# Performance work log

Measured on AMD Instinct MI355X. Metric: run time of the kernel, lower is better.

Reference implementation:

```python
import jax, jax.numpy as jnp
import numpy as np

D_MODEL, D_STATE, EXPAND = 1024, 16, 2
D_INNER = D_MODEL * EXPAND
BATCH, SEQ = 4, 2048
DT = 0.1

def setup_inputs() -> dict:
    key = jax.random.key(0)
    ks = jax.random.split(key, 12)
    s = 0.02
    inp = {
        "x": jax.random.normal(ks[0], (BATCH, SEQ, D_MODEL), jnp.float32),
        "B_mod": jax.random.normal(ks[1], (BATCH, D_STATE), jnp.float32) * 0.1,
        "C_mod": jax.random.normal(ks[2], (BATCH, D_STATE), jnp.float32) * 0.1,
        "W_in": jax.random.normal(ks[3], (D_MODEL, 2 * D_INNER), jnp.float32) * s,
        "b_in": jnp.zeros((2 * D_INNER,), jnp.float32),
        "conv_w": jax.random.normal(ks[4], (D_INNER, 1, 3), jnp.float32) * 0.3,
        "conv_b": jnp.zeros((D_INNER,), jnp.float32),
        "A_log": jnp.tile(jnp.log(jnp.arange(1, D_STATE + 1, dtype=jnp.float32))[None, :], (D_INNER, 1)),
        "D": jnp.ones((D_INNER,), jnp.float32),
        "W_B": jax.random.normal(ks[5], (D_INNER, D_STATE), jnp.float32) * s,
        "b_B": jnp.zeros((D_STATE,), jnp.float32),
        "W_C": jax.random.normal(ks[6], (D_INNER, D_STATE), jnp.float32) * s,
        "b_C": jnp.zeros((D_STATE,), jnp.float32),
        "W_out": jax.random.normal(ks[7], (D_INNER, D_MODEL), jnp.float32) * s,
        "b_out": jnp.zeros((D_MODEL,), jnp.float32),
    }
    return inp

def _silu(v):
    return v * jax.nn.sigmoid(v)

def reference(x, B_mod, C_mod, W_in, b_in, conv_w, conv_b, A_log, D, W_B, b_B, W_C, b_C, W_out, b_out):
    # in_proj + split + gate
    xr = x @ W_in + b_in                      # (B, L, 2*D_INNER)
    x_ssm, x_res = jnp.split(xr, 2, axis=-1)
    x_ssm = _silu(x_ssm)
    # depthwise conv1d, kernel 3, padding 1
    xc = jnp.transpose(x_ssm, (0, 2, 1))      # (B, C, L)
    xc = jax.lax.conv_general_dilated(
        xc, conv_w, window_strides=(1,), padding=[(1, 1)],
        dimension_numbers=("NCH", "OIH", "NCH"), feature_group_count=D_INNER)
    xc = xc + conv_b[None, :, None]
    x_ssm = jnp.transpose(xc, (0, 2, 1))      # (B, L, D_INNER)
    # SSM params
    A = -jnp.exp(A_log)                       # (D_INNER, D_STATE)
    A_bar = jnp.exp(A * DT)
    B = x_ssm @ W_B + b_B + B_mod[:, None, :] # (B, L, D_STATE)
    C = x_ssm @ W_C + b_C + C_mod[:, None, :]
    # sequential scan over time
    def step(h, inp):
        xt, Bt, Ct = inp                      # (B,D_INNER), (B,S), (B,S)
        h = A_bar[None] * h + xt[:, :, None] * Bt[:, None, :]
        yt = jnp.einsum("bds,bs->bd", h, Ct)
        return h, yt
    h0 = jnp.zeros((x.shape[0], D_INNER, D_STATE), x.dtype)
    xs = (jnp.moveaxis(x_ssm, 1, 0), jnp.moveaxis(B, 1, 0), jnp.moveaxis(C, 1, 0))
    _, ys = jax.lax.scan(step, h0, xs)        # (L, B, D_INNER)
    y = jnp.moveaxis(ys, 0, 1) + D[None, None, :] * x_ssm
    y = y * _silu(x_res)
    return y @ W_out + b_out
```

## Files before the change

### kernel.cpp

```cpp
#include <hip/hip_runtime.h>
#include <stdint.h>

#define D_MODEL 1024
#define D_STATE 16
#define D_INNER 2048
#define BATCH   4
#define SEQ     2048
#define ML      (BATCH*SEQ)
#define CH      64
#define NCHUNK  (SEQ/CH)
#define KSEG    8

typedef unsigned short u16;
typedef u16   u16x8  __attribute__((ext_vector_type(8)));
typedef short s16x8  __attribute__((ext_vector_type(8)));
typedef float f32x4  __attribute__((ext_vector_type(4)));

__device__ __forceinline__ float b2f(u16 u){
  union { uint32_t i; float f; } v; v.i = ((uint32_t)u) << 16; return v.f;
}
__device__ __forceinline__ u16 f2b(float f){
  uint32_t x = __float_as_uint(f);
  return (u16)((x + 0x7fffu + ((x >> 16) & 1u)) >> 16);
}
__device__ __forceinline__ float silu_f(float v){
  return v / (1.f + __expf(-v));
}
__device__ __forceinline__ void gl_lds16(const void* gp, void* lp){
  __builtin_amdgcn_global_load_lds(
      (const __attribute__((address_space(1))) void*)gp,
      (__attribute__((address_space(3))) void*)lp, 16, 0, 0);
}

__global__ __launch_bounds__(256) void prep_k(const float* __restrict__ W_in,
                                              const float* __restrict__ W_out,
                                              const float* __restrict__ x,
                                              const float* __restrict__ W_B,
                                              const float* __restrict__ W_C,
                                              u16* __restrict__ Wt_in,
                                              u16* __restrict__ Wt_out,
                                              u16* __restrict__ xbf,
                                              u16* __restrict__ Wt_bc){
  __shared__ float tile[32][33];
  int bb = blockIdx.x;
  if (bb < 6144) {
    const float* in; u16* out; int R, C, bx, by;
    if (bb < 4096) { in = W_in;  out = Wt_in;  R = 1024; C = 4096;
                     bx = (bb & 127) * 32; by = (bb >> 7) * 32; }
    else { bb -= 4096; in = W_out; out = Wt_out; R = 2048; C = 1024;
                     bx = (bb & 31) * 32; by = (bb >> 5) * 32; }
    int tx = threadIdx.x & 31, ty = threadIdx.x >> 5;
    #pragma unroll
    for (int i = 0; i < 32; i += 8)
      tile[ty + i][tx] = in[(size_t)(by + ty + i) * C + bx + tx];
    __syncthreads();
    #pragma unroll
    for (int i = 0; i < 32; i += 8)
      out[(size_t)(bx + ty + i) * R + by + tx] = f2b(tile[tx][ty + i]);
  } else if (bb < 10240) {
    bb -= 6144;
    size_t i = ((size_t)bb * 256 + threadIdx.x) * 8;
    f32x4 a = *(const f32x4*)(x + i);
    f32x4 b = *(const f32x4*)(x + i + 4);
    u16x8 o;
    #pragma unroll
    for (int j = 0; j < 4; ++j){ o[j] = f2b(a[j]); o[4+j] = f2b(b[j]); }
    *(u16x8*)(xbf + i) = o;
  } else {
    bb -= 10240;
    int n = bb >> 3;
    int k = (bb & 7) * 256 + threadIdx.x;
    const float* src = (n < 16) ? W_B : W_C;
    Wt_bc[(size_t)n * D_INNER + k] = f2b(src[(size_t)k * 16 + (n & 15)]);
  }
}

#define G1_K  1024
#define G1_NT (G1_K/64)

__global__ __launch_bounds__(512, 2) void gemm1_k(const u16* __restrict__ A,
                                                  const u16* __restrict__ Bt,
                                                  const float* __restrict__ bias,
                                                  u16* __restrict__ out0,
                                                  u16* __restrict__ out1){
  __shared__ __align__(16) u16 ldsAll[256*264];
  u16* ldsA = ldsAll;
  u16* ldsB = ldsAll + 4*8192;

  const int bid = blockIdx.x;
  const int xcd = bid & 7, t2 = bid >> 3;
  const int n0 = (xcd*2 + (t2 & 1)) * 256;
  const int m0 = (t2 >> 1) * 256;

  const int tid  = threadIdx.x;
  const int wave = tid >> 6, lane = tid & 63;
  const int wr = wave >> 2;
  const int wc = wave & 3;
  const int lrow = lane & 15;
  const int q    = lane >> 4;

  const int cx0  = ((q ^ (lrow & 7)) << 3);
  const int cx1  = cx0 ^ 32;
  const int arow = lrow * 64;

  const int srow = lane >> 3;
  const int scol = (((lane & 7) ^ (lane >> 3)) << 3);

  auto stageA = [&](int buf, int h, int k0){
    const u16* s = A + (size_t)(m0 + h*128 + wave*16 + srow) * G1_K + k0 + scol;
    u16* d = ldsA + (buf*2 + h)*8192 + wave*1024;
    gl_lds16(s,                  d);
    gl_lds16(s + (size_t)8*G1_K, d + 512);
  };
  auto stageB = [&](int buf, int h, int k0){
    const u16* s = Bt + (size_t)(n0 + h*128 + wave*16 + srow) * G1_K + k0 + scol;
    u16* d = ldsB + (buf*2 + h)*8192 + wave*1024;
    gl_lds16(s,                  d);
    gl_lds16(s + (size_t)8*G1_K, d + 512);
  };

  f32x4 acc[8][4];
  #pragma unroll
  for (int i = 0; i < 8; ++i)
    #pragma unroll
    for (int j = 0; j < 4; ++j) acc[i][j] = (f32x4){0.f,0.f,0.f,0.f};

  s16x8 aA[2][2], aB[2][2];
  s16x8 bX[4][2], bY[4][2];

  #define READ_AQ(dst, Q, nb)                                            \
    { const u16* p_ = ldsA + ((nb)*2 + wr)*8192 + (Q)*2048 + arow;       \
      dst[0][0] = *(const s16x8*)(p_ + cx0);                             \
      dst[0][1] = *(const s16x8*)(p_ + cx1);                             \
      dst[1][0] = *(const s16x8*)(p_ + 1024 + cx0);                      \
      dst[1][1] = *(const s16x8*)(p_ + 1024 + cx1); }
  #define READ_B8(dst, nb)                                               \
    { const u16* p_ = ldsB + ((nb)*2 + (wc>>1))*8192 + (wc&1)*4096 + arow; \
      _Pragma("unroll")                                                  \
      for (int nj_ = 0; nj_ < 4; ++nj_){                                 \
        dst[nj_][0] = *(const s16x8*)(p_ + nj_*1024 + cx0);              \
        dst[nj_][1] = *(const s16x8*)(p_ + nj_*1024 + cx1); } }
  #define MFMA_Q(Q, AF, BF)                                              \
    { _Pragma("unroll")                                                  \
      for (int nj_ = 0; nj_ < 4; ++nj_){                                 \
        _Pragma("unroll")                                                \
        for (int kk_ = 0; kk_ < 2; ++kk_){                               \
          acc[2*(Q)][nj_]   = __builtin_amdgcn_mfma_f32_16x16x32_bf16(AF[0][kk_], BF[nj_][kk_], acc[2*(Q)][nj_],   0,0,0); \
          acc[2*(Q)+1][nj_] = __builtin_amdgcn_mfma_f32_16x16x32_bf16(AF[1][kk_], BF[nj_][kk_], acc[2*(Q)+1][nj_], 0,0,0); } } }

  stageA(0,0,0); stageA(0,1,0); stageB(0,0,0); stageB(0,1,0);
  stageB(1,0,64); stageB(1,1,64);
  asm volatile("s_waitcnt vmcnt(4)" ::: "memory");
  __builtin_amdgcn_s_barrier();
  __builtin_amdgcn_sched_barrier(0);
  READ_B8(bX, 0);
  READ_AQ(aA, 0, 0);

  auto tile_body = [&](int tt, int buf, s16x8 (&bC)[4][2], s16x8 (&bN)[4][2]){
    const int k1 = (tt+1 < G1_NT ? tt+1 : G1_NT-1) * 64;
    const int k2 = (tt+2 < G1_NT ? tt+2 : G1_NT-1) * 64;
    const int nb = buf ^ 1;

    READ_AQ(aB, 1, buf);
    stageA(nb, 1, k1);
    stageA(nb, 0, k1);
    __builtin_amdgcn_s_barrier();
    asm volatile("s_waitcnt lgkmcnt(4)" ::: "memory");
    __builtin_amdgcn_sched_barrier(0);
    __builtin_amdgcn_s_setprio(1);
    MFMA_Q(0, aA, bC);
    __builtin_amdgcn_s_setprio(0);
    __builtin_amdgcn_s_barrier();

    READ_AQ(aA, 2, buf);
    stageB(buf, 0, k2);
    __builtin_amdgcn_s_barrier();
    asm volatile("s_waitcnt lgkmcnt(4)" ::: "memory");
    __builtin_amdgcn_sched_barrier(0);
    __builtin_amdgcn_s_setprio(1);
    MFMA_Q(1, aB, bC);
    __builtin_amdgcn_s_setprio(0);
    __builtin_amdgcn_s_barrier();

    READ_AQ(aB, 3, buf);
    stageB(buf, 1, k2);
    __builtin_amdgcn_s_barrier();
    asm volatile("s_waitcnt lgkmcnt(4)" ::: "memory");
    __builtin_amdgcn_sched_barrier(0);
    __builtin_amdgcn_s_setprio(1);
    MFMA_Q(2, aA, bC);
    __builtin_amdgcn_s_setprio(0);
    __builtin_amdgcn_s_barrier();

    asm volatile("s_waitcnt vmcnt(4)" ::: "memory");
    __builtin_amdgcn_s_barrier();
    __builtin_amdgcn_sched_barrier(0);
    READ_B8(bN, nb);
    READ_AQ(aA, 0, nb);
    asm volatile("s_waitcnt lgkmcnt(12)" ::: "memory");
    __builtin_amdgcn_sched_barrier(0);
    __builtin_amdgcn_s_setprio(1);
    MFMA_Q(3, aB, bC);
    __builtin_amdgcn_s_setprio(0);
    __builtin_amdgcn_s_barrier();
  };

  for (int tt2 = 0; tt2 < G1_NT; tt2 += 2) {
    tile_body(tt2,     0, bX, bY);
    tile_body(tt2 + 1, 1, bY, bX);
  }

  asm volatile("s_waitcnt vmcnt(0)" ::: "memory");
  __syncthreads();

  #pragma unroll
  for (int nj = 0; nj < 4; ++nj) {
    const int colg = n0 + wc*64 + nj*16 + lrow;
    const float bv = bias[colg];
    const int coll = wc*64 + nj*16 + lrow;
    #pragma unroll
    for (int mi = 0; mi < 8; ++mi) {
      #pragma unroll
      for (int r = 0; r < 4; ++r) {
        const int rowl = wr*128 + mi*16 + q*4 + r;
        ldsAll[rowl*264 + coll] = f2b(silu_f(acc[mi][nj][r] + bv));
      }
    }
  }
  __syncthreads();

  u16* op = (n0 < D_INNER) ? out0 : out1;
  const int colbase = n0 & (D_INNER - 1);
  #pragma unroll
  for (int it = 0; it < 16; ++it) {
    const int f   = it*512 + tid;
    const int row = f >> 5;
    const int ch  = f & 31;
    u16x8 v = *(const u16x8*)(ldsAll + row*264 + ch*8);
    *(u16x8*)(op + (size_t)(m0 + row)*D_INNER + colbase + ch*8) = v;
  }
  #undef READ_AQ
  #undef READ_B8
  #undef MFMA_Q
}

template<int MODE>
__global__ __launch_bounds__(256) void gemm_bt(const u16* __restrict__ A,
                                               const u16* __restrict__ Bt,
                                               const float* __restrict__ bias,
                                               u16* __restrict__ out0,
                                               u16* __restrict__ out1,
                                               float* __restrict__ outf,
                                               int M, int N, int K, int n_per_xcd){
  __shared__ __align__(16) u16 Asb[2][128*32];
  __shared__ __align__(16) u16 Bsb[2][128*32];
  const int bid = blockIdx.x;
  const int xcd = bid & 7, t2 = bid >> 3;
  const int n0 = (xcd * n_per_xcd + (t2 % n_per_xcd)) * 128;
  const int m0 = (t2 / n_per_xcd) * 128;
  const int t    = threadIdx.x;
  const int wave = t >> 6, lane = t & 63;
  const int wm   = (wave >> 1) * 64, wn = (wave & 1) * 64;
  const int lrow = lane & 15, kq = (lane >> 4) * 8;
  const int srow = lane >> 2;
  const int scol = (lane & 3) * 8;

  f32x4 acc[4][4];
  #pragma unroll
  for (int i = 0; i < 4; ++i)
    #pragma unroll
    for (int j = 0; j < 4; ++j)
      acc[i][j] = (f32x4){0.f, 0.f, 0.f, 0.f};

  auto stage = [&](int buf, int k0){
    #pragma unroll
    for (int i = 0; i < 2; ++i) {
      int R0 = (wave*2 + i) * 16;
      gl_lds16(&A [(size_t)(m0 + R0 + srow)*K + k0 + scol], &Asb[buf][R0*32]);
      gl_lds16(&Bt[(size_t)(n0 + R0 + srow)*K + k0 + scol], &Bsb[buf][R0*32]);
    }
  };

  const int KT = K >> 5;
  stage(0, 0);
  __syncthreads();
  for (int kt = 0; kt < KT; ++kt) {
    const int cur = kt & 1;
    if (kt + 1 < KT) stage(1 - cur, (kt + 1) * 32);
    s16x8 af[4], bfr[4];
    #pragma unroll
    for (int i = 0; i < 4; ++i) af[i]  = *(const s16x8*)&Asb[cur][(wm + i*16 + lrow)*32 + kq];
    #pragma unroll
    for (int j = 0; j < 4; ++j) bfr[j] = *(const s16x8*)&Bsb[cur][(wn + j*16 + lrow)*32 + kq];
    #pragma unroll
    for (int i = 0; i < 4; ++i)
      #pragma unroll
      for (int j = 0; j < 4; ++j)
        acc[i][j] = __builtin_amdgcn_mfma_f32_16x16x32_bf16(af[i], bfr[j], acc[i][j], 0, 0, 0);
    __syncthreads();
  }

  const int Nh = N >> 1;
  #pragma unroll
  for (int i = 0; i < 4; ++i) {
    #pragma unroll
    for (int j = 0; j < 4; ++j) {
      int col = n0 + wn + j*16 + lrow;
      float bv = bias[col];
      #pragma unroll
      for (int r = 0; r < 4; ++r) {
        int row = m0 + wm + i*16 + (lane >> 4)*4 + r;
        float v = acc[i][j][r] + bv;
        if (MODE == 0) {
          outf[(size_t)row * N + col] = v;
        } else {
          float s = silu_f(v);
          if (col < Nh) out0[(size_t)row * Nh + col]        = f2b(s);
          else          out1[(size_t)row * Nh + (col - Nh)] = f2b(s);
        }
      }
    }
  }
}

__global__ __launch_bounds__(256) void bc_gemm_k(const u16* __restrict__ xs,
                                                 const float* __restrict__ conv_w,
                                                 const float* __restrict__ conv_b,
                                                 const u16* __restrict__ Wt,
                                                 float* __restrict__ partial){
  __shared__ __align__(16) u16 Rsb[130*40];
  __shared__ __align__(16) u16 Asb[128*40];
  __shared__ __align__(16) u16 Wsb[32*40];
  const int kseg = blockIdx.x;
  const int m0   = blockIdx.y * 128;
  const int t    = threadIdx.x;
  const int wave = t >> 6, lane = t & 63;
  const int wm   = wave * 32;
  const int lrow = lane & 15, kq = (lane >> 4) * 8;
  const bool zfirst = (m0 & (SEQ-1)) == 0;
  const bool zlast  = ((m0+128) & (SEQ-1)) == 0;
  const int ccol = t & 31, r0c = (t >> 5) * 16;

  f32x4 acc[2][2];
  #pragma unroll
  for (int i = 0; i < 2; ++i)
    #pragma unroll
    for (int j = 0; j < 2; ++j)
      acc[i][j] = (f32x4){0.f, 0.f, 0.f, 0.f};

  const int kbase = kseg * (D_INNER / KSEG);
  for (int ks = 0; ks < (D_INNER / KSEG); ks += 32) {
    int k0 = kbase + ks;
    if (t < 128) {
      int f = t * 8;
      int r = f >> 5, c = f & 31;
      *(u16x8*)&Wsb[r*40 + c] = *(const u16x8*)&Wt[(size_t)r*D_INNER + k0 + c];
    }
    #pragma unroll
    for (int i = 0; i < 3; ++i) {
      int idx = i*256 + t;
      if (idx < 520) {
        int r = idx >> 2, c = (idx & 3) * 8;
        u16x8 v = (u16x8){0,0,0,0,0,0,0,0};
        bool zero = (r == 0 && zfirst) || (r == 129 && zlast);
        if (!zero)
          v = *(const u16x8*)&xs[(size_t)(m0 - 1 + r)*D_INNER + k0 + c];
        *(u16x8*)&Rsb[r*40 + c] = v;
      }
    }
    __syncthreads();
    {
      const int dcol = k0 + ccol;
      const float cw0 = conv_w[dcol*3], cw1 = conv_w[dcol*3+1], cw2 = conv_w[dcol*3+2];
      const float cbv = conv_b[dcol];
      #pragma unroll
      for (int r = 0; r < 16; ++r) {
        int rr = r0c + r;
        float v = cw0 * b2f(Rsb[rr*40 + ccol])
                + cw1 * b2f(Rsb[(rr+1)*40 + ccol])
                + cw2 * b2f(Rsb[(rr+2)*40 + ccol]) + cbv;
        Asb[rr*40 + ccol] = f2b(v);
      }
    }
    __syncthreads();
    s16x8 af[2], wf[2];
    #pragma unroll
    for (int i = 0; i < 2; ++i) af[i] = *(const s16x8*)&Asb[(wm + i*16 + lrow)*40 + kq];
    #pragma unroll
    for (int j = 0; j < 2; ++j) wf[j] = *(const s16x8*)&Wsb[(j*16 + lrow)*40 + kq];
    #pragma unroll
    for (int i = 0; i < 2; ++i)
      #pragma unroll
      for (int j = 0; j < 2; ++j)
        acc[i][j] = __builtin_amdgcn_mfma_f32_16x16x32_bf16(af[i], wf[j], acc[i][j], 0, 0, 0);
    __syncthreads();
  }

  #pragma unroll
  for (int i = 0; i < 2; ++i)
    #pragma unroll
    for (int j = 0; j < 2; ++j)
      #pragma unroll
      for (int r = 0; r < 4; ++r) {
        int row = m0 + wm + i*16 + (lane >> 4)*4 + r;
        int col = j*16 + lrow;
        partial[((size_t)kseg * ML + row) * 32 + col] = acc[i][j][r];
      }
}

__global__ __launch_bounds__(256) void bc_reduce_k(const float* __restrict__ partial,
    const float* __restrict__ b_B, const float* __restrict__ B_mod,
    const float* __restrict__ b_C, const float* __restrict__ C_mod,
    float* __restrict__ Bbuf, float* __restrict__ Cbuf){
  int g = blockIdx.x * 256 + threadIdx.x;
  int row = g >> 5, col = g & 31;
  int b = row >> 11;
  float s = 0.f;
  #pragma unroll
  for (int seg = 0; seg < KSEG; ++seg)
    s += partial[(size_t)seg * ML * 32 + g];
  if (col < 16) Bbuf[(size_t)row*16 + col]      = s + b_B[col]      + B_mod[b*16 + col];
  else          Cbuf[(size_t)row*16 + col - 16] = s + b_C[col - 16] + C_mod[b*16 + col - 16];
}

__global__ __launch_bounds__(256) void state_k(const u16* __restrict__ xs,
    const float* __restrict__ conv_w, const float* __restrict__ conv_b,
    const float* __restrict__ Bbuf, const float* __restrict__ A_log,
    float* __restrict__ hend){
  int c = blockIdx.x, db = blockIdx.y, b = blockIdx.z;
  int d = db*256 + threadIdx.x;

  float Abar[16];
  #pragma unroll
  for (int s = 0; s < 16; ++s)
    Abar[s] = __expf(-0.1f * __expf(A_log[d*16 + s]));
  float h[16];
  #pragma unroll
  for (int s = 0; s < 16; ++s) h[s] = 0.f;

  const float w0 = conv_w[d*3], w1 = conv_w[d*3+1], w2 = conv_w[d*3+2], cb = conv_b[d];
  size_t base = (size_t)b * SEQ * D_INNER + (size_t)c * CH * D_INNER + d;
  const float* Br = Bbuf + ((size_t)b * SEQ + (size_t)c * CH) * 16;
  const int l0 = c * CH;

  float xm = (l0 > 0) ? b2f(xs[base - D_INNER]) : 0.f;
  float x0 = b2f(xs[base]);
  float xp = b2f(xs[base + D_INNER]);
  float Bc[16];
  #pragma unroll
  for (int s = 0; s < 16; ++s) Bc[s] = Br[s];

  for (int l = 0; l < CH; ++l){
    float xq = 0.f;
    if (l0 + l + 2 < SEQ) xq = b2f(xs[base + (size_t)(l+2)*D_INNER]);
    float Bl[16];
    #pragma unroll
    for (int s = 0; s < 16; ++s) Bl[s] = Bc[s];
    if (l < CH-1){
      #pragma unroll
      for (int s = 0; s < 16; ++s) Bc[s] = Br[(l+1)*16 + s];
    }
    float xc = w0*xm + w1*x0 + w2*xp + cb;
    #pragma unroll
    for (int s = 0; s < 16; ++s)
      h[s] = Abar[s]*h[s] + xc*Bl[s];
    xm = x0; x0 = xp; xp = xq;
  }
  float* hp = hend + (((size_t)(b*NCHUNK + c))*D_INNER + d)*16;
  #pragma unroll
  for (int q = 0; q < 4; ++q)
    *(f32x4*)(hp + q*4) = (f32x4){h[q*4], h[q*4+1], h[q*4+2], h[q*4+3]};
}

__global__ __launch_bounds__(256) void prefix_k(const float* __restrict__ hend,
    const float* __restrict__ A_log, float* __restrict__ hin){
  int g = blockIdx.x*256 + threadIdx.x;
  int s = g & 15;
  int d = (g >> 4) & (D_INNER-1);
  int b = g >> 15;
  float decay = __expf(-0.1f * (float)CH * __expf(A_log[d*16 + s]));
  size_t stride = (size_t)D_INNER * 16;
  const float* he = hend + (size_t)b*NCHUNK*stride + (size_t)d*16 + s;
  float*       hi = hin  + (size_t)b*NCHUNK*stride + (size_t)d*16 + s;
  float h = 0.f;
  for (int c0 = 0; c0 < NCHUNK; c0 += 8){
    float v[8];
    #pragma unroll
    for (int i = 0; i < 8; ++i) v[i] = he[(size_t)(c0+i)*stride];
    #pragma unroll
    for (int i = 0; i < 8; ++i){
      hi[(size_t)(c0+i)*stride] = h;
      h = decay*h + v[i];
    }
  }
}

__global__ __launch_bounds__(256) void scan2_k(const u16* __restrict__ xs,
    const u16* __restrict__ gate,
    const float* __restrict__ conv_w, const float* __restrict__ conv_b,
    const float* __restrict__ Bbuf, const float* __restrict__ Cbuf,
    const float* __restrict__ A_log, const float* __restrict__ Dp,
    const float* __restrict__ hin, u16* __restrict__ ybuf){
  int c = blockIdx.x, db = blockIdx.y, b = blockIdx.z;
  int d = db*256 + threadIdx.x;

  float Abar[16];
  #pragma unroll
  for (int s = 0; s < 16; ++s)
    Abar[s] = __expf(-0.1f * __expf(A_log[d*16 + s]));
  float h[16];
  const float* hp = hin + (((size_t)(b*NCHUNK + c))*D_INNER + d)*16;
  #pragma unroll
  for (int q = 0; q < 4; ++q){
    f32x4 v = *(const f32x4*)(hp + q*4);
    #pragma unroll
    for (int j = 0; j < 4; ++j) h[q*4 + j] = v[j];
  }
  float Dd = Dp[d];
  const float w0 = conv_w[d*3], w1 = conv_w[d*3+1], w2 = conv_w[d*3+2], cb = conv_b[d];

  size_t base = (size_t)b * SEQ * D_INNER + (size_t)c * CH * D_INNER + d;
  const float* Br = Bbuf + ((size_t)b * SEQ + (size_t)c * CH) * 16;
  const float* Cr = Cbuf + ((size_t)b * SEQ + (size_t)c * CH) * 16;
  const int l0 = c * CH;

  float xm = (l0 > 0) ? b2f(xs[base - D_INNER]) : 0.f;
  float x0 = b2f(xs[base]);
  float xp = b2f(xs[base + D_INNER]);
  float Bc[16], Cc[16];
  #pragma unroll
  for (int s = 0; s < 16; ++s){ Bc[s] = Br[s]; Cc[s] = Cr[s]; }
  float gcur = b2f(gate[base]);

  for (int l = 0; l < CH; ++l){
    float xq = 0.f;
    if (l0 + l + 2 < SEQ) xq = b2f(xs[base + (size_t)(l+2)*D_INNER]);
    float gnext = (l < CH-1) ? b2f(gate[base + (size_t)(l+1)*D_INNER]) : 0.f;
    float Bl[16], Cl[16];
    #pragma unroll
    for (int s = 0; s < 16; ++s){ Bl[s] = Bc[s]; Cl[s] = Cc[s]; }
    if (l < CH-1){
      #pragma unroll
      for (int s = 0; s < 16; ++s){ Bc[s] = Br[(l+1)*16 + s]; Cc[s] = Cr[(l+1)*16 + s]; }
    }
    float xc = w0*xm + w1*x0 + w2*xp + cb;
    float ya[4] = {0.f, 0.f, 0.f, 0.f};
    #pragma unroll
    for (int s = 0; s < 16; ++s){
      float hv = Abar[s]*h[s] + xc*Bl[s];
      h[s] = hv;
      ya[s & 3] += hv * Cl[s];
    }
    float y = ((ya[0]+ya[1]) + (ya[2]+ya[3]) + Dd*xc) * gcur;
    ybuf[base + (size_t)l*D_INNER] = f2b(y);
    xm = x0; x0 = xp; xp = xq; gcur = gnext;
  }
}

extern "C" void kernel_launch(void* const* d_in, const int* in_sizes, int n_in,
                              void* d_out, int out_size, void* d_ws, size_t ws_size,
                              hipStream_t stream){
  const float* x      = (const float*)d_in[0];
  const float* B_mod  = (const float*)d_in[1];
  const float* C_mod  = (const float*)d_in[2];
  const float* W_in   = (const float*)d_in[3];
  const float* b_in   = (const float*)d_in[4];
  const float* conv_w = (const float*)d_in[5];
  const float* conv_b = (const float*)d_in[6];
  const float* A_log  = (const float*)d_in[7];
  const float* Dp     = (const float*)d_in[8];
  const float* W_B    = (const float*)d_in[9];
  const float* b_B    = (const float*)d_in[10];
  const float* W_C    = (const float*)d_in[11];
  const float* b_C    = (const float*)d_in[12];
  const float* W_out  = (const float*)d_in[13];
  const float* b_out  = (const float*)d_in[14];
  float* out = (float*)d_out;

  char* ws = (char*)d_ws;
  size_t off = 0;
  auto alloc = [&](size_t bytes)->char* {
    char* p = ws + off; off += (bytes + 255) & ~(size_t)255; return p;
  };
  u16* Wt_in  = (u16*)alloc((size_t)(2*D_INNER)*D_MODEL*2);
  u16* Wt_out = (u16*)alloc((size_t)D_MODEL*D_INNER*2);
  u16* xs     = (u16*)alloc((size_t)ML*D_INNER*2);
  u16* gatep  = (u16*)alloc((size_t)ML*D_INNER*2);
  u16* ybuf   = (u16*)alloc((size_t)ML*D_INNER*2);
  float* Bbuf = (float*)alloc((size_t)ML*D_STATE*4);
  float* Cbuf = (float*)alloc((size_t)ML*D_STATE*4);
  u16* xbf    = (u16*)alloc((size_t)ML*D_MODEL*2);
  float* hin  = (float*)alloc((size_t)BATCH*NCHUNK*D_INNER*16*4);
  u16* Wt_bc  = (u16*)alloc((size_t)32*D_INNER*2);
  float* hend    = (float*)xbf;
  float* partial = (float*)Wt_in;

  prep_k<<<dim3(10496), 256, 0, stream>>>(W_in, W_out, x, W_B, W_C,
                                          Wt_in, Wt_out, xbf, Wt_bc);

  gemm1_k<<<dim3(512), 512, 0, stream>>>(xbf, Wt_in, b_in, xs, gatep);

  bc_gemm_k<<<dim3(KSEG, ML/128), 256, 0, stream>>>(xs, conv_w, conv_b, Wt_bc, partial);
  bc_reduce_k<<<dim3((ML*32)/256), 256, 0, stream>>>(
      partial, b_B, B_mod, b_C, C_mod, Bbuf, Cbuf);

  state_k<<<dim3(NCHUNK, D_INNER/256, BATCH), 256, 0, stream>>>(
      xs, conv_w, conv_b, Bbuf, A_log, hend);
  prefix_k<<<dim3((BATCH*D_INNER*16)/256), 256, 0, stream>>>(hend, A_log, hin);
  scan2_k<<<dim3(NCHUNK, D_INNER/256, BATCH), 256, 0, stream>>>(
      xs, gatep, conv_w, conv_b, Bbuf, Cbuf, A_log, Dp, hin, ybuf);

  gemm_bt<0><<<dim3(512), 256, 0, stream>>>(
      ybuf, Wt_out, b_out, nullptr, nullptr, out, ML, D_MODEL, D_INNER, 1);
}
```

Measured before the change: 370.8 us.

## Replace 256x256 ping-pong in_proj GEMM with simpler 256x128 tile, higher occupancy

The in_proj GEMM kernel drops its hand-scheduled 256x256 tile with quarter-step interleaving, setprio and explicit waitcnts. It now uses a 256x128 tile with K-step 32, a plain double-buffered loop synchronised by one __syncthreads per step, and a launch bound of 4 blocks per CU. The grid doubles to 1024 blocks, and the epilogue writes the output through LDS in two halves to fit the smaller shared buffer. The aim is to hide latency through occupancy rather than manual scheduling. The cost is less reuse per tile, more barriers, and a short K-step that may expose load latency.

Result: faster. 359.0 us (-3.2%).

```diff
diff --git a/kernel.cpp b/kernel.cpp
--- a/kernel.cpp
+++ b/kernel.cpp
@@ -76,172 +76,101 @@
 }
 
 #define G1_K  1024
-#define G1_NT (G1_K/64)
-
-__global__ __launch_bounds__(512, 2) void gemm1_k(const u16* __restrict__ A,
+
+__global__ __launch_bounds__(512, 4) void gemm1_k(const u16* __restrict__ A,
                                                   const u16* __restrict__ Bt,
                                                   const float* __restrict__ bias,
                                                   u16* __restrict__ out0,
                                                   u16* __restrict__ out1){
-  __shared__ __align__(16) u16 ldsAll[256*264];
-  u16* ldsA = ldsAll;
-  u16* ldsB = ldsAll + 4*8192;
+  __shared__ __align__(16) u16 lds[24576];
+  u16* ldsA = lds;
+  u16* ldsB = lds + 16384;
 
   const int bid = blockIdx.x;
   const int xcd = bid & 7, t2 = bid >> 3;
-  const int n0 = (xcd*2 + (t2 & 1)) * 256;
-  const int m0 = (t2 >> 1) * 256;
+  const int n0 = (xcd*4 + (t2 & 3)) * 128;
+  const int m0 = (t2 >> 2) * 256;
 
   const int tid  = threadIdx.x;
   const int wave = tid >> 6, lane = tid & 63;
-  const int wr = wave >> 2;
-  const int wc = wave & 3;
+  const int wr = wave >> 1;
+  const int wn = (wave & 1) * 64;
   const int lrow = lane & 15;
   const int q    = lane >> 4;
 
-  const int cx0  = ((q ^ (lrow & 7)) << 3);
-  const int cx1  = cx0 ^ 32;
-  const int arow = lrow * 64;
-
-  const int srow = lane >> 3;
-  const int scol = (((lane & 7) ^ (lane >> 3)) << 3);
-
-  auto stageA = [&](int buf, int h, int k0){
-    const u16* s = A + (size_t)(m0 + h*128 + wave*16 + srow) * G1_K + k0 + scol;
-    u16* d = ldsA + (buf*2 + h)*8192 + wave*1024;
-    gl_lds16(s,                  d);
-    gl_lds16(s + (size_t)8*G1_K, d + 512);
+  const int cxa  = (q ^ (lrow & 3)) << 3;
+  const int srow = lane >> 2;
+  const int schunk = (((lane & 3) ^ (srow & 3)) << 3);
+
+  auto stageA = [&](int buf, int k0){
+    const u16* s = A + (size_t)(m0 + wave*32 + srow) * G1_K + k0 + schunk;
+    u16* d = ldsA + buf*8192 + wave*1024;
+    gl_lds16(s,                   d);
+    gl_lds16(s + (size_t)16*G1_K, d + 512);
   };
-  auto stageB = [&](int buf, int h, int k0){
-    const u16* s = Bt + (size_t)(n0 + h*128 + wave*16 + srow) * G1_K + k0 + scol;
-    u16* d = ldsB + (buf*2 + h)*8192 + wave*1024;
-    gl_lds16(s,                  d);
-    gl_lds16(s + (size_t)8*G1_K, d + 512);
+  auto stageB = [&](int buf, int k0){
+    const u16* s = Bt + (size_t)(n0 + wave*16 + srow) * G1_K + k0 + schunk;
+    gl_lds16(s, ldsB + buf*4096 + wave*512);
   };
 
-  f32x4 acc[8][4];
-  #pragma unroll
-  for (int i = 0; i < 8; ++i)
+  f32x4 acc[4][4];
+  #pragma unroll
+  for (int i = 0; i < 4; ++i)
     #pragma unroll
     for (int j = 0; j < 4; ++j) acc[i][j] = (f32x4){0.f,0.f,0.f,0.f};
 
-  s16x8 aA[2][2], aB[2][2];
-  s16x8 bX[4][2], bY[4][2];
-
-  #define READ_AQ(dst, Q, nb)                                            \
-    { const u16* p_ = ldsA + ((nb)*2 + wr)*8192 + (Q)*2048 + arow;       \
-      dst[0][0] = *(const s16x8*)(p_ + cx0);                             \
-      dst[0][1] = *(const s16x8*)(p_ + cx1);                             \
-      dst[1][0] = *(const s16x8*)(p_ + 1024 + cx0);                      \
-      dst[1][1] = *(const s16x8*)(p_ + 1024 + cx1); }
-  #define READ_B8(dst, nb)                                               \
-    { const u16* p_ = ldsB + ((nb)*2 + (wc>>1))*8192 + (wc&1)*4096 + arow; \
-      _Pragma("unroll")                                                  \
-      for (int nj_ = 0; nj_ < 4; ++nj_){                                 \
-        dst[nj_][0] = *(const s16x8*)(p_ + nj_*1024 + cx0);              \
-        dst[nj_][1] = *(const s16x8*)(p_ + nj_*1024 + cx1); } }
-  #define MFMA_Q(Q, AF, BF)                                              \
-    { _Pragma("unroll")                                                  \
-      for (int nj_ = 0; nj_ < 4; ++nj_){                                 \
-        _Pragma("unroll")                                                \
-        for (int kk_ = 0; kk_ < 2; ++kk_){                               \
-          acc[2*(Q)][nj_]   = __builtin_amdgcn_mfma_f32_16x16x32_bf16(AF[0][kk_], BF[nj_][kk_], acc[2*(Q)][nj_],   0,0,0); \
-          acc[2*(Q)+1][nj_] = __builtin_amdgcn_mfma_f32_16x16x32_bf16(AF[1][kk_], BF[nj_][kk_], acc[2*(Q)+1][nj_], 0,0,0); } } }
-
-  stageA(0,0,0); stageA(0,1,0); stageB(0,0,0); stageB(0,1,0);
-  stageB(1,0,64); stageB(1,1,64);
-  asm volatile("s_waitcnt vmcnt(4)" ::: "memory");
-  __builtin_amdgcn_s_barrier();
-  __builtin_amdgcn_sched_barrier(0);
-  READ_B8(bX, 0);
-  READ_AQ(aA, 0, 0);
-
-  auto tile_body = [&](int tt, int buf, s16x8 (&bC)[4][2], s16x8 (&bN)[4][2]){
-    const int k1 = (tt+1 < G1_NT ? tt+1 : G1_NT-1) * 64;
-    const int k2 = (tt+2 < G1_NT ? tt+2 : G1_NT-1) * 64;
-    const int nb = buf ^ 1;
-
-    READ_AQ(aB, 1, buf);
-    stageA(nb, 1, k1);
-    stageA(nb, 0, k1);
-    __builtin_amdgcn_s_barrier();
-    asm volatile("s_waitcnt lgkmcnt(4)" ::: "memory");
-    __builtin_amdgcn_sched_barrier(0);
-    __builtin_amdgcn_s_setprio(1);
-    MFMA_Q(0, aA, bC);
-    __builtin_amdgcn_s_setprio(0);
-    __builtin_amdgcn_s_barrier();
-
-    READ_AQ(aA, 2, buf);
-    stageB(buf, 0, k2);
-    __builtin_amdgcn_s_barrier();
-    asm volatile("s_waitcnt lgkmcnt(4)" ::: "memory");
-    __builtin_amdgcn_sched_barrier(0);
-    __builtin_amdgcn_s_setprio(1);
-    MFMA_Q(1, aB, bC);
-    __builtin_amdgcn_s_setprio(0);
-    __builtin_amdgcn_s_barrier();
-
-    READ_AQ(aB, 3, buf);
-    stageB(buf, 1, k2);
-    __builtin_amdgcn_s_barrier();
-    asm volatile("s_waitcnt lgkmcnt(4)" ::: "memory");
-    __builtin_amdgcn_sched_barrier(0);
-    __builtin_amdgcn_s_setprio(1);
-    MFMA_Q(2, aA, bC);
-    __builtin_amdgcn_s_setprio(0);
-    __builtin_amdgcn_s_barrier();
-
-    asm volatile("s_waitcnt vmcnt(4)" ::: "memory");
-    __builtin_amdgcn_s_barrier();
-    __builtin_amdgcn_sched_barrier(0);
-    READ_B8(bN, nb);
-    READ_AQ(aA, 0, nb);
-    asm volatile("s_waitcnt lgkmcnt(12)" ::: "memory");
-    __builtin_amdgcn_sched_barrier(0);
-    __builtin_amdgcn_s_setprio(1);
-    MFMA_Q(3, aB, bC);
-    __builtin_amdgcn_s_setprio(0);
-    __builtin_amdgcn_s_barrier();
-  };
-
-  for (int tt2 = 0; tt2 < G1_NT; tt2 += 2) {
-    tile_body(tt2,     0, bX, bY);
-    tile_body(tt2 + 1, 1, bY, bX);
-  }
-
-  asm volatile("s_waitcnt vmcnt(0)" ::: "memory");
+  stageA(0, 0); stageB(0, 0);
   __syncthreads();
 
-  #pragma unroll
-  for (int nj = 0; nj < 4; ++nj) {
-    const int colg = n0 + wc*64 + nj*16 + lrow;
-    const float bv = bias[colg];
-    const int coll = wc*64 + nj*16 + lrow;
-    #pragma unroll
-    for (int mi = 0; mi < 8; ++mi) {
-      #pragma unroll
-      for (int r = 0; r < 4; ++r) {
-        const int rowl = wr*128 + mi*16 + q*4 + r;
-        ldsAll[rowl*264 + coll] = f2b(silu_f(acc[mi][nj][r] + bv));
-      }
-    }
-  }
-  __syncthreads();
+  const int KT = G1_K / 32;
+  for (int kt = 0; kt < KT; ++kt) {
+    const int cur = kt & 1;
+    if (kt + 1 < KT) { stageA(1 - cur, (kt+1)*32); stageB(1 - cur, (kt+1)*32); }
+    s16x8 af[4], bf[4];
+    #pragma unroll
+    for (int mi = 0; mi < 4; ++mi)
+      af[mi] = *(const s16x8*)&ldsA[cur*8192 + (wr*64 + mi*16 + lrow)*32 + cxa];
+    #pragma unroll
+    for (int nj = 0; nj < 4; ++nj)
+      bf[nj] = *(const s16x8*)&ldsB[cur*4096 + (wn + nj*16 + lrow)*32 + cxa];
+    #pragma unroll
+    for (int mi = 0; mi < 4; ++mi)
+      #pragma unroll
+      for (int nj = 0; nj < 4; ++nj)
+        acc[mi][nj] = __builtin_amdgcn_mfma_f32_16x16x32_bf16(af[mi], bf[nj], acc[mi][nj], 0,0,0);
+    __syncthreads();
+  }
 
   u16* op = (n0 < D_INNER) ? out0 : out1;
   const int colbase = n0 & (D_INNER - 1);
   #pragma unroll
-  for (int it = 0; it < 16; ++it) {
-    const int f   = it*512 + tid;
-    const int row = f >> 5;
-    const int ch  = f & 31;
-    u16x8 v = *(const u16x8*)(ldsAll + row*264 + ch*8);
-    *(u16x8*)(op + (size_t)(m0 + row)*D_INNER + colbase + ch*8) = v;
-  }
-  #undef READ_AQ
-  #undef READ_B8
-  #undef MFMA_Q
+  for (int h = 0; h < 2; ++h) {
+    __syncthreads();
+    if ((wr >> 1) == h) {
+      const int rbase = (wr & 1) * 64;
+      #pragma unroll
+      for (int nj = 0; nj < 4; ++nj) {
+        const int col = wn + nj*16 + lrow;
+        const float bv = bias[n0 + col];
+        #pragma unroll
+        for (int mi = 0; mi < 4; ++mi) {
+          #pragma unroll
+          for (int r = 0; r < 4; ++r) {
+            const int row = rbase + mi*16 + q*4 + r;
+            lds[row*136 + col] = f2b(silu_f(acc[mi][nj][r] + bv));
+          }
+        }
+      }
+    }
+    __syncthreads();
+    #pragma unroll
+    for (int it = 0; it < 4; ++it) {
+      const int f = it*512 + tid;
+      const int row = f >> 4, ch = f & 15;
+      u16x8 v = *(const u16x8*)&lds[row*136 + ch*8];
+      *(u16x8*)(op + (size_t)(m0 + h*128 + row)*D_INNER + colbase + ch*8) = v;
+    }
+  }
 }
 
 template<int MODE>
@@ -598,7 +527,7 @@
   prep_k<<<dim3(10496), 256, 0, stream>>>(W_in, W_out, x, W_B, W_C,
                                           Wt_in, Wt_out, xbf, Wt_bc);
 
-  gemm1_k<<<dim3(512), 512, 0, stream>>>(xbf, Wt_in, b_in, xs, gatep);
+  gemm1_k<<<dim3(1024), 512, 0, stream>>>(xbf, Wt_in, b_in, xs, gatep);
 
   bc_gemm_k<<<dim3(KSEG, ML/128), 256, 0, stream>>>(xs, conv_w, conv_b, Wt_bc, partial);
   bc_reduce_k<<<dim3((ML*32)/256), 256, 0, stream>>>(
```
